# Kernel tuning notes

Hardware: AMD Instinct MI355X
Metric: run time of the kernel (lower is better)

## Reference

```python
import jax, jax.numpy as jnp
import numpy as np

Q = 127.0  # int8 symmetric quantization range


def _round_ste(v):
    # straight-through rounding (forward: round; backward: identity)
    return v + jax.lax.stop_gradient(jnp.round(v) - v)


def quantize_rowwise(x):
    # per-row absmax int8 quantization: returns int8-valued float tensor + row scale
    absmax = jnp.max(jnp.abs(x), axis=1, keepdims=True)  # [N,1]
    q = jnp.clip(_round_ste(x * (Q / absmax)), -Q, Q)
    return q, absmax


def quantize_global(w):
    # whole-tensor absmax int8 quantization
    absmax = jnp.max(jnp.abs(w))
    q = jnp.clip(_round_ste(w * (Q / absmax)), -Q, Q)
    return q, absmax


def int8_matmul_dequant_bias(a_q, b_q_t, state_a, state_b, bias):
    # a_q: [N,K] int8-valued, b_q_t: [K,M]; dequant = state_a*state_b/(127*127)
    acc = jnp.matmul(a_q, b_q_t)  # int8-valued floats -> exact small-int products
    return acc * (state_a * state_b / (Q * Q)) + bias


def setup_inputs() -> dict:
    key = jax.random.key(0)
    k1, k2, k3, k4, k5 = jax.random.split(key, 5)
    B, S, D, H = 4, 2048, 2048, 8192
    x = jax.random.normal(k1, (B, S, D), dtype=jnp.float32)
    W1 = jax.random.normal(k2, (H, D), dtype=jnp.float32) * (1.0 / np.sqrt(D))
    B1 = jax.random.normal(k3, (H,), dtype=jnp.float32) * 0.02
    W2 = jax.random.normal(k4, (D, H), dtype=jnp.float32) * (1.0 / np.sqrt(H))
    B2 = jax.random.normal(k5, (D,), dtype=jnp.float32) * 0.02
    return {"x": x, "W1": W1, "B1": B1, "W2": W2, "B2": B2}


def reference(x, W1, B1, W2, B2):
    X1 = x.reshape(-1, x.shape[-1])  # [N, D]
    X1_q, sX1 = quantize_rowwise(X1)
    W1_q, sW1 = quantize_global(W1)
    X2_pre = int8_matmul_dequant_bias(X1_q, W1_q.T, sX1, sW1, B1)  # [N, H]
    X2 = jax.nn.gelu(X2_pre, approximate=True)  # fused gelu in original kernel
    X2_q, sX2 = quantize_rowwise(X2)
    W2_q, sW2 = quantize_global(W2)
    out = int8_matmul_dequant_bias(X2_q, W2_q.T, sX2, sW2, B2)  # [N, D]
    return out.reshape(*x.shape[:-1], -1)
```

## Files before the change

### kernel.cpp

```cpp
#include <hip/hip_runtime.h>
#include <cstdint>
#include <cstddef>


typedef int v4i __attribute__((ext_vector_type(4)));

#define AS1 __attribute__((address_space(1)))
#define AS3 __attribute__((address_space(3)))

#define WAIT_LGKM(N) asm volatile("s_waitcnt lgkmcnt(" #N ")" ::: "memory")
#define WAIT_VM(N)   asm volatile("s_waitcnt vmcnt(" #N ")" ::: "memory")
#define SBAR() __builtin_amdgcn_s_barrier()
#define SFENCE() __builtin_amdgcn_sched_barrier(0)

__device__ __forceinline__ void gload_lds16(const void* g, void* l) {
    __builtin_amdgcn_global_load_lds((const AS1 void*)g, (AS3 void*)l, 16, 0, 0);
}

__device__ __forceinline__ float absmax4(float4 v, float cur) {
    return fmaxf(cur, fmaxf(fmaxf(fabsf(v.x), fabsf(v.y)),
                            fmaxf(fabsf(v.z), fabsf(v.w))));
}

__device__ __forceinline__ int quant1(float x, float inv) {
    int q = (int)rintf(x * inv);
    return min(127, max(-127, q));
}

__device__ __forceinline__ uint32_t quant4(float4 v, float inv) {
    uint32_t b0 = (uint32_t)(uint8_t)(int8_t)quant1(v.x, inv);
    uint32_t b1 = (uint32_t)(uint8_t)(int8_t)quant1(v.y, inv);
    uint32_t b2 = (uint32_t)(uint8_t)(int8_t)quant1(v.z, inv);
    uint32_t b3 = (uint32_t)(uint8_t)(int8_t)quant1(v.w, inv);
    return b0 | (b1 << 8) | (b2 << 16) | (b3 << 24);
}

__global__ __launch_bounds__(256) void wabs_kernel(
    const float* __restrict__ W, int n4, float* __restrict__ out)
{
    int tid = blockIdx.x * 256 + threadIdx.x;
    int stride = gridDim.x * 256;
    const float4* W4 = (const float4*)W;
    float amax = 0.0f;
    for (int i = tid; i < n4; i += stride) amax = absmax4(W4[i], amax);
    #pragma unroll
    for (int off = 32; off >= 1; off >>= 1)
        amax = fmaxf(amax, __shfl_xor(amax, off));
    __shared__ float red[4];
    if ((threadIdx.x & 63) == 0) red[threadIdx.x >> 6] = amax;
    __syncthreads();
    if (threadIdx.x == 0) {
        amax = fmaxf(fmaxf(red[0], red[1]), fmaxf(red[2], red[3]));
        atomicMax((int*)out, __float_as_int(amax));
    }
}

__global__ __launch_bounds__(256) void wquant_kernel(
    const float* __restrict__ W, int n4, const float* __restrict__ s,
    uint32_t* __restrict__ Wq)
{
    float inv = 127.0f / s[0];
    int tid = blockIdx.x * 256 + threadIdx.x;
    int stride = gridDim.x * 256;
    const float4* W4 = (const float4*)W;
    for (int i = tid; i < n4; i += stride) Wq[i] = quant4(W4[i], inv);
}

template<int CNT>
__global__ __launch_bounds__(256) void rowquant_kernel(
    const float* __restrict__ X, int8_t* __restrict__ Xq,
    float* __restrict__ rowAbs)
{
    const int row = blockIdx.x;
    const int t = threadIdx.x;
    const size_t cols = (size_t)CNT * 1024;
    const float4* Xr = (const float4*)(X + (size_t)row * cols);
    float4 vals[CNT];
    float amax = 0.0f;
    #pragma unroll
    for (int j = 0; j < CNT; j++) {
        vals[j] = Xr[j * 256 + t];
        amax = absmax4(vals[j], amax);
    }
    #pragma unroll
    for (int off = 32; off >= 1; off >>= 1)
        amax = fmaxf(amax, __shfl_xor(amax, off));
    __shared__ float red[4];
    if ((t & 63) == 0) red[t >> 6] = amax;
    __syncthreads();
    amax = fmaxf(fmaxf(red[0], red[1]), fmaxf(red[2], red[3]));
    if (t == 0) rowAbs[row] = amax;
    float inv = 127.0f / amax;
    uint32_t* out = (uint32_t*)(Xq + (size_t)row * cols);
    #pragma unroll
    for (int j = 0; j < CNT; j++) out[j * 256 + t] = quant4(vals[j], inv);
}

template<int GELU>
__global__ __launch_bounds__(512, 2) void gemm8_i8(
    const int8_t* __restrict__ A, const int8_t* __restrict__ B,
    int K, int Ncols, int nbx,
    const float* __restrict__ rowScale, const float* __restrict__ wScale,
    const float* __restrict__ bias, float* __restrict__ Cout)
{
    extern __shared__ int8_t lds[];
    int8_t* AsB = lds;
    int8_t* BsB = lds + 65536;

    const int nwg = gridDim.x;
    const int bid = blockIdx.x;
    const int wg = (bid & 7) * (nwg >> 3) + (bid >> 3);
    const int bx = wg % nbx;
    const int by = wg / nbx;
    const int brow = by * 256;
    const int bcol = bx * 256;

    const int t = threadIdx.x;
    const int lane = t & 63;
    const int w = t >> 6;
    const int wr = w >> 2;
    const int wc = w & 3;
    const int llo = lane & 15;
    const int lhi = lane >> 4;

    const int8_t* gA = A + (size_t)brow * K;
    const int8_t* gB = B + (size_t)bcol * K;

    const int rq = t >> 3;
    const int sl = (t & 7) ^ (rq & 7);
    const size_t srcOffBase = (size_t)rq * K + (size_t)sl * 16;
    const int ldsDst = t * 16;

    const int aRow = (wr * 128 + llo) * 128;
    const int bRow = (wc * 64 + llo) * 128;
    const int s0 = ((lhi) ^ (llo & 7)) * 16;
    const int s1 = ((4 + lhi) ^ (llo & 7)) * 16;

    const int NT = K >> 7;

    v4i acc[8][4] = {};

    auto stage = [&](int halfId, int par, int srcTile) {
        const int8_t* g = (halfId >= 2) ? gB : gA;
        int8_t* ldsOp = (halfId >= 2) ? BsB : AsB;
        const int hh = halfId & 1;
        const size_t gb = (size_t)(hh * 128) * (size_t)K
                        + (size_t)srcTile * 128 + srcOffBase;
        int8_t* d = ldsOp + par * 32768 + hh * 16384 + ldsDst;
        gload_lds16(g + gb, d);
        gload_lds16(g + gb + (size_t)64 * K, d + 8192);
    };

    {
        const int t1 = NT > 1 ? 1 : 0;
        stage(0, 0, 0); stage(1, 0, 0); stage(2, 0, 0); stage(3, 0, 0);
        stage(0, 1, t1);
    }
    WAIT_VM(2);
    SFENCE();
    SBAR();

    #define MFMA16(AV, BV, MOFF)                                            \
        __builtin_amdgcn_s_setprio(1);                                      \
        _Pragma("unroll")                                                   \
        for (int m = 0; m < 4; m++)                                         \
            _Pragma("unroll")                                               \
            for (int n = 0; n < 4; n++)                                     \
                acc[MOFF + m][n] = __builtin_amdgcn_mfma_i32_16x16x64_i8(   \
                    AV[m], BV[n], acc[MOFF + m][n], 0, 0, 0);               \
        __builtin_amdgcn_s_setprio(0);

    for (int T = 0; T < NT; ++T) {
        const int buf = T & 1;
        const int8_t* Ab = AsB + buf * 32768;
        const int8_t* Bb = BsB + buf * 32768;
        const int tn  = (T + 1 < NT) ? T + 1 : T;
        const int tn2 = (T + 2 < NT) ? T + 2 : T;
        const int parN = (T + 1) & 1;

        v4i aA[4], aB_[4], aC[4], aD[4], b0[4], b1[4];

        #pragma unroll
        for (int m = 0; m < 4; m++) aA[m] = *(const v4i*)(Ab + aRow + m * 2048 + s0);
        #pragma unroll
        for (int n = 0; n < 4; n++) b0[n] = *(const v4i*)(Bb + bRow + n * 2048 + s0);
        stage(1, parN, tn);
        SBAR();
        WAIT_LGKM(0);
        SFENCE();
        MFMA16(aA, b0, 0)
        SBAR();

        #pragma unroll
        for (int m = 0; m < 4; m++) aB_[m] = *(const v4i*)(Ab + aRow + 8192 + m * 2048 + s0);
        #pragma unroll
        for (int n = 0; n < 4; n++) b1[n] = *(const v4i*)(Bb + bRow + n * 2048 + s1);
        #pragma unroll
        for (int m = 0; m < 4; m++) aC[m] = *(const v4i*)(Ab + aRow + m * 2048 + s1);
        stage(2, parN, tn);
        SBAR();
        WAIT_LGKM(8);
        SFENCE();
        MFMA16(aB_, b0, 4)
        SBAR();

        #pragma unroll
        for (int m = 0; m < 4; m++) aD[m] = *(const v4i*)(Ab + aRow + 8192 + m * 2048 + s1);
        stage(3, parN, tn);
        SBAR();
        WAIT_LGKM(0);
        SFENCE();
        MFMA16(aC, b1, 0)
        SBAR();

        stage(0, buf, tn2);
        MFMA16(aD, b1, 4)
        WAIT_VM(2);
        SFENCE();
        SBAR();
    }
    #undef MFMA16

    const float wsc = wScale[0] * (1.0f / (127.0f * 127.0f));
    #pragma unroll
    for (int m = 0; m < 8; m++) {
        #pragma unroll
        for (int r4 = 0; r4 < 4; r4++) {
            const int row = brow + wr * 128 + m * 16 + lhi * 4 + r4;
            const float s = rowScale[row] * wsc;
            #pragma unroll
            for (int n = 0; n < 4; n++) {
                const int col = bcol + wc * 64 + n * 16 + llo;
                float v = (float)acc[m][n][r4] * s + bias[col];
                if (GELU) {
                    float u = v + 0.044715f * v * v * v;
                    v = v / (1.0f + __expf(-1.5957691216057308f * u));
                }
                Cout[(size_t)row * Ncols + col] = v;
            }
        }
    }
}

extern "C" void kernel_launch(void* const* d_in, const int* in_sizes, int n_in,
                              void* d_out, int out_size, void* d_ws, size_t ws_size,
                              hipStream_t stream)
{
    const float* x  = (const float*)d_in[0];
    const float* W1 = (const float*)d_in[1];
    const float* B1 = (const float*)d_in[2];
    const float* W2 = (const float*)d_in[3];
    const float* B2 = (const float*)d_in[4];
    float* out = (float*)d_out;

    const int N = 8192, D = 2048, H = 8192;
    const size_t MB = 1024 * 1024;

    hipFuncSetAttribute((const void*)gemm8_i8<1>,
                        hipFuncAttributeMaxDynamicSharedMemorySize, 131072);
    hipFuncSetAttribute((const void*)gemm8_i8<0>,
                        hipFuncAttributeMaxDynamicSharedMemorySize, 131072);

    char* ws = (char*)d_ws;
    float* sW1 = (float*)(ws + 0);
    float* sW2 = (float*)(ws + 4);
    float* sX1 = (float*)(ws + 256);
    float* sX2 = (float*)(ws + 256 + 32768);
    size_t off = 1 * MB;
    int8_t* X1q = (int8_t*)(ws + off);
    int8_t* W2q = X1q;
    off += (size_t)N * D;
    int8_t* W1q = (int8_t*)(ws + off); off += (size_t)H * D;
    int8_t* X2q = (int8_t*)(ws + off); off += (size_t)N * H;
    float*  X2f = (float*)(ws + off);
    const size_t fixedBytes = off;

    int chunk = N;
    if (ws_size < fixedBytes + (size_t)N * H * 4) {
        size_t avail = ws_size > fixedBytes ? ws_size - fixedBytes : 0;
        size_t c = avail / ((size_t)H * 4);
        c = (c / 256) * 256;
        if (c < 256) c = 256;
        if (c > (size_t)N) c = N;
        chunk = (int)c;
    }

    hipMemsetAsync(d_ws, 0, 256 + 65536, stream);

    wabs_kernel<<<2048, 256, 0, stream>>>(W1, H * D / 4, sW1);
    wquant_kernel<<<4096, 256, 0, stream>>>(W1, H * D / 4, sW1, (uint32_t*)W1q);
    rowquant_kernel<2><<<N, 256, 0, stream>>>(x, X1q, sX1);

    for (int r0 = 0; r0 < N; r0 += chunk) {
        const int rows = min(chunk, N - r0);
        gemm8_i8<1><<<(H / 256) * (rows / 256), 512, 131072, stream>>>(
            X1q + (size_t)r0 * D, W1q, D, H, H / 256,
            sX1 + r0, sW1, B1, X2f);
        rowquant_kernel<8><<<rows, 256, 0, stream>>>(
            X2f, X2q + (size_t)r0 * H, sX2 + r0);
    }

    wabs_kernel<<<2048, 256, 0, stream>>>(W2, D * H / 4, sW2);
    wquant_kernel<<<4096, 256, 0, stream>>>(W2, D * H / 4, sW2, (uint32_t*)W2q);

    gemm8_i8<0><<<(D / 256) * (N / 256), 512, 131072, stream>>>(
        X2q, W2q, H, D, D / 256, sX2, sW2, B2, out);
}
```

Before: 619.5 us.

## Switch int8 GEMM mainloop to K=64 tiles with four-stage LDS ring buffer

The main loop now walks K in 64-wide tiles instead of 128 and keeps a four-slot LDS ring, prefetching three tiles ahead rather than double-buffering. The swizzle and LDS addressing are recomputed for the 64-byte row layout. Each iteration does two MFMA phases instead of four, with fewer barriers per iteration but twice as many iterations. The aim is deeper prefetch so global-load latency is better hidden, at the cost of more loop overhead and shorter MFMA bursts between barriers.

```diff
diff --git a/kernel.cpp b/kernel.cpp
--- a/kernel.cpp
+++ b/kernel.cpp
@@ -126,37 +126,33 @@
     const int8_t* gA = A + (size_t)brow * K;
     const int8_t* gB = B + (size_t)bcol * K;
 
-    const int rq = t >> 3;
-    const int sl = (t & 7) ^ (rq & 7);
-    const size_t srcOffBase = (size_t)rq * K + (size_t)sl * 16;
+    const size_t srcOffBase = (size_t)(t >> 2) * K
+                            + (size_t)(((t & 3) ^ ((t >> 3) & 3)) * 16);
     const int ldsDst = t * 16;
 
-    const int aRow = (wr * 128 + llo) * 128;
-    const int bRow = (wc * 64 + llo) * 128;
-    const int s0 = ((lhi) ^ (llo & 7)) * 16;
-    const int s1 = ((4 + lhi) ^ (llo & 7)) * 16;
-
-    const int NT = K >> 7;
+    const int sA = ((lhi ^ ((llo >> 1) & 3)) << 4);
+    const int aOff = (wr * 128 + llo) * 64 + sA;
+    const int bOff = (wc * 64 + llo) * 64 + sA;
+
+    const int NT = K >> 6;
 
     v4i acc[8][4] = {};
 
-    auto stage = [&](int halfId, int par, int srcTile) {
-        const int8_t* g = (halfId >= 2) ? gB : gA;
-        int8_t* ldsOp = (halfId >= 2) ? BsB : AsB;
-        const int hh = halfId & 1;
-        const size_t gb = (size_t)(hh * 128) * (size_t)K
-                        + (size_t)srcTile * 128 + srcOffBase;
-        int8_t* d = ldsOp + par * 32768 + hh * 16384 + ldsDst;
-        gload_lds16(g + gb, d);
-        gload_lds16(g + gb + (size_t)64 * K, d + 8192);
+    auto stageA = [&](int srcTile) {
+        const size_t gb = (size_t)srcTile * 64 + srcOffBase;
+        int8_t* d = AsB + (srcTile & 3) * 16384 + ldsDst;
+        gload_lds16(gA + gb, d);
+        gload_lds16(gA + gb + (size_t)128 * K, d + 8192);
     };
-
-    {
-        const int t1 = NT > 1 ? 1 : 0;
-        stage(0, 0, 0); stage(1, 0, 0); stage(2, 0, 0); stage(3, 0, 0);
-        stage(0, 1, t1);
-    }
-    WAIT_VM(2);
+    auto stageB = [&](int srcTile) {
+        const size_t gb = (size_t)srcTile * 64 + srcOffBase;
+        int8_t* d = BsB + (srcTile & 3) * 16384 + ldsDst;
+        gload_lds16(gB + gb, d);
+        gload_lds16(gB + gb + (size_t)128 * K, d + 8192);
+    };
+
+    stageA(0); stageB(0); stageA(1); stageB(1); stageA(2); stageB(2);
+    WAIT_VM(8);
     SFENCE();
     SBAR();
 
@@ -171,55 +167,37 @@
         __builtin_amdgcn_s_setprio(0);
 
     for (int T = 0; T < NT; ++T) {
-        const int buf = T & 1;
-        const int8_t* Ab = AsB + buf * 32768;
-        const int8_t* Bb = BsB + buf * 32768;
-        const int tn  = (T + 1 < NT) ? T + 1 : T;
-        const int tn2 = (T + 2 < NT) ? T + 2 : T;
-        const int parN = (T + 1) & 1;
-
-        v4i aA[4], aB_[4], aC[4], aD[4], b0[4], b1[4];
-
-        #pragma unroll
-        for (int m = 0; m < 4; m++) aA[m] = *(const v4i*)(Ab + aRow + m * 2048 + s0);
-        #pragma unroll
-        for (int n = 0; n < 4; n++) b0[n] = *(const v4i*)(Bb + bRow + n * 2048 + s0);
-        stage(1, parN, tn);
+        const int buf = T & 3;
+        const int8_t* Ab = AsB + buf * 16384;
+        const int8_t* Bb = BsB + buf * 16384;
+        const int ts = (T + 3 < NT) ? T + 3 : NT - 1;
+        v4i a0[4], a1[4], bb[4];
+
+        #pragma unroll
+        for (int m = 0; m < 4; m++) a0[m] = *(const v4i*)(Ab + aOff + m * 1024);
+        #pragma unroll
+        for (int n = 0; n < 4; n++) bb[n] = *(const v4i*)(Bb + bOff + n * 1024);
+        stageA(ts);
         SBAR();
         WAIT_LGKM(0);
         SFENCE();
-        MFMA16(aA, b0, 0)
-        SBAR();
-
-        #pragma unroll
-        for (int m = 0; m < 4; m++) aB_[m] = *(const v4i*)(Ab + aRow + 8192 + m * 2048 + s0);
-        #pragma unroll
-        for (int n = 0; n < 4; n++) b1[n] = *(const v4i*)(Bb + bRow + n * 2048 + s1);
-        #pragma unroll
-        for (int m = 0; m < 4; m++) aC[m] = *(const v4i*)(Ab + aRow + m * 2048 + s1);
-        stage(2, parN, tn);
-        SBAR();
-        WAIT_LGKM(8);
-        SFENCE();
-        MFMA16(aB_, b0, 4)
-        SBAR();
-
-        #pragma unroll
-        for (int m = 0; m < 4; m++) aD[m] = *(const v4i*)(Ab + aRow + 8192 + m * 2048 + s1);
-        stage(3, parN, tn);
+        MFMA16(a0, bb, 0)
+        SBAR();
+
+        #pragma unroll
+        for (int m = 0; m < 4; m++) a1[m] = *(const v4i*)(Ab + aOff + 4096 + m * 1024);
+        stageB(ts);
         SBAR();
         WAIT_LGKM(0);
         SFENCE();
-        MFMA16(aC, b1, 0)
-        SBAR();
-
-        stage(0, buf, tn2);
-        MFMA16(aD, b1, 4)
-        WAIT_VM(2);
+        MFMA16(a1, bb, 4)
+        WAIT_VM(8);
         SFENCE();
         SBAR();
     }
     #undef MFMA16
+
+    WAIT_VM(0);
 
     const float wsc = wScale[0] * (1.0f / (127.0f * 127.0f));
     #pragma unroll
```

Result: no change. 628.0 us (+1.4%).
